# Kernel optimization log

Hardware: AMD Instinct MI355X
Metric: run time of the kernel (lower is better)

Reference implementation:

```python
import jax, jax.numpy as jnp
import numpy as np

BATCH = 4        # opt.batch_size
NPATCH = 4096    # patches per batch element
DIM = 256        # feature dim
MAXC = 5         # self.max_classes
T = 0.07         # opt.nce_T
NEG_FILL = -10.0


def setup_inputs() -> dict:
    key = jax.random.key(0)
    k1, k2, k3 = jax.random.split(key, 3)
    N = BATCH * NPATCH
    features_src = jax.random.normal(k1, (N, DIM), jnp.float32)
    features_tgt = jax.random.normal(k2, (N, DIM), jnp.float32)
    classes = jax.random.randint(k3, (N,), 0, MAXC, dtype=jnp.int32)
    return {"features_src": features_src, "features_tgt": features_tgt, "classes": classes}


def reference(features_src, features_tgt, classes):
    # feat_k = feat_k.detach()
    tgt = jax.lax.stop_gradient(features_tgt)

    # positive logits: per-row dot product, divided by temperature
    pos = jnp.sum(features_src * tgt, axis=-1) / T            # [N]

    src_b = features_src.reshape(BATCH, NPATCH, DIM)
    tgt_b = tgt.reshape(BATCH, NPATCH, DIM)
    cls = classes.reshape(BATCH, NPATCH)

    # full negative logit matrix per batch element
    logits = jnp.einsum('bnd,bmd->bnm', src_b, tgt_b)         # [B, n, n]
    same = cls[:, :, None] == cls[:, None, :]                 # [B, n, n] same-class mask

    # per-class smallest negative logit: min over (row in class c, col not in class c)
    row_min = jnp.min(jnp.where(same, jnp.inf, logits), axis=2)          # [B, n]
    class_eq = cls[:, :, None] == jnp.arange(MAXC)[None, None, :]        # [B, n, C]
    class_min = jnp.min(jnp.where(class_eq, row_min[:, :, None], jnp.inf), axis=1)  # [B, C]
    smallest = jnp.minimum(class_min, NEG_FILL) / T                      # [B, C]
    counts = jnp.sum(class_eq, axis=1)                                   # [B, C]

    # per-row pad value and pad multiplicity (num_pairs_should - num_pairs_is = count_c - 1)
    sm_row = jnp.take_along_axis(smallest, cls, axis=1)                  # [B, n]
    npad = jnp.take_along_axis(counts, cls, axis=1) - 1                  # [B, n]

    # logsumexp over [pos, negatives (other classes only), npad copies of smallest]
    lse_neg = jax.nn.logsumexp(jnp.where(same, -jnp.inf, logits / T), axis=2)  # [B, n]
    pad_term = jnp.where(npad > 0,
                         jnp.log(jnp.maximum(npad, 1).astype(jnp.float32)) + sm_row,
                         -jnp.inf)
    pos_b = pos.reshape(BATCH, NPATCH)
    lse = jax.nn.logsumexp(jnp.stack([pos_b, lse_neg, pad_term], axis=-1), axis=-1)
    loss = lse - pos_b                                                   # CE with label 0

    # match torch ordering: rows concatenated per batch, grouped by class (stable)
    order = jnp.argsort(cls, axis=1)  # jnp.argsort is stable
    return jnp.take_along_axis(loss, order, axis=1).reshape(-1)
```

## Files before the change

### kernel.cpp

```cpp
#include <hip/hip_runtime.h>
#include <cstdint>

#define NBATCH 4
#define NPATCH 4096
#define MAXC   5
#define BM 64
#define BN 64
#define NSPLIT 8
#define SPLITCOLS (NPATCH / NSPLIT)
#define NCIT (SPLITCOLS / BN)
#define SCALE  14.285714285714286f
#define SCALE2 20.609929006188747f
#define LN2F   0.6931471805599453f
#define NEGH  -1.0e38f
#define NEGFILL_T -142.85714285714286f
#define NROWS (NBATCH * NPATCH)

typedef __attribute__((ext_vector_type(8))) short short8;
typedef __attribute__((ext_vector_type(4))) float f32x4;

__device__ __forceinline__ float fexp2(float x) { return __builtin_amdgcn_exp2f(x); }
__device__ __forceinline__ float flog2(float x) { return __builtin_amdgcn_logf(x); }

__device__ __forceinline__ unsigned short f2bf(float f) {
  uint32_t u = __builtin_bit_cast(uint32_t, f);
  u = (u + 0x7FFFu + ((u >> 16) & 1u)) >> 16;
  return (unsigned short)u;
}


__global__ __launch_bounds__(256) void k_aux(const float* __restrict__ src,
                                             const float* __restrict__ tgt,
                                             const int* __restrict__ classes,
                                             unsigned short* __restrict__ tgtb,
                                             unsigned short* __restrict__ srcb,
                                             float* __restrict__ pos,
                                             int* __restrict__ outpos,
                                             int* __restrict__ counts) {
  int blk = blockIdx.x;
  if (blk < NROWS / 4) {
    int row  = blk * 4 + (threadIdx.x >> 6);
    int lane = threadIdx.x & 63;
    float4 va = ((const float4*)src)[(size_t)row * 64 + lane];
    float4 vb = ((const float4*)tgt)[(size_t)row * 64 + lane];
    float d = va.x * vb.x + va.y * vb.y + va.z * vb.z + va.w * vb.w;
#pragma unroll
    for (int off = 32; off > 0; off >>= 1) d += __shfl_xor(d, off, 64);
    if (lane == 0) pos[row] = d * SCALE;
    return;
  }
  if (blk < NROWS / 4 + 1024) {
    int which = (blk - NROWS / 4) >> 9;
    int fb = (blk - NROWS / 4) & 511;
    const float* in = which ? src : tgt;
    unsigned short* outb = which ? srcb : tgtb;
    float sc = which ? SCALE2 : 1.0f;
    int t  = threadIdx.x;
    int tl = fb * 2 + (t >> 7);
    int tt = t & 127;
    int row16 = tt >> 3;
    int kg    = tt & 7;
    const float4* rp = (const float4*)(in + (size_t)(tl * 16 + row16) * 256 + kg * 32);
    uint4* wp = (uint4*)outb + (size_t)tl * 512 + (size_t)(kg * 4) * 16 + row16;
#pragma unroll
    for (int j = 0; j < 4; ++j) {
      float4 fa = rp[j * 2];
      float4 fb2 = rp[j * 2 + 1];
      union { ushort4 h[2]; uint4 u; } pk;
      pk.h[0].x = f2bf(fa.x * sc);  pk.h[0].y = f2bf(fa.y * sc);
      pk.h[0].z = f2bf(fa.z * sc);  pk.h[0].w = f2bf(fa.w * sc);
      pk.h[1].x = f2bf(fb2.x * sc); pk.h[1].y = f2bf(fb2.y * sc);
      pk.h[1].z = f2bf(fb2.z * sc); pk.h[1].w = f2bf(fb2.w * sc);
      wp[j * 16] = pk.u;
    }
    return;
  }

  __shared__ int sa[MAXC * 256];
  __shared__ int sb2[MAXC * 256];
  int b = blk - (NROWS / 4 + 1024), t = threadIdx.x;
  int base = b * NPATCH + t * 16;
  int cv[16];
#pragma unroll
  for (int e = 0; e < 16; ++e) cv[e] = classes[base + e];
  int cnt[MAXC];
#pragma unroll
  for (int c = 0; c < MAXC; ++c) {
    cnt[c] = 0;
#pragma unroll
    for (int e = 0; e < 16; ++e)
      if (cv[e] == c) cnt[c]++;
  }
#pragma unroll
  for (int c = 0; c < MAXC; ++c) sa[c * 256 + t] = cnt[c];
  __syncthreads();

  int* rp = sa; int* wp = sb2;
  for (int d = 1; d < 256; d <<= 1) {
#pragma unroll
    for (int c = 0; c < MAXC; ++c) {
      int v = rp[c * 256 + t];
      if (t >= d) v += rp[c * 256 + t - d];
      wp[c * 256 + t] = v;
    }
    __syncthreads();
    int* tmp = rp; rp = wp; wp = tmp;
  }

  int tot[MAXC], excl[MAXC], off[MAXC + 1];
  off[0] = 0;
#pragma unroll
  for (int c = 0; c < MAXC; ++c) {
    tot[c]  = rp[c * 256 + 255];
    excl[c] = rp[c * 256 + t] - cnt[c];
    off[c + 1] = off[c] + tot[c];
  }
#pragma unroll
  for (int c = 0; c < MAXC; ++c) {
    int r = off[c] + excl[c];
#pragma unroll
    for (int e = 0; e < 16; ++e)
      if (cv[e] == c) { outpos[base + e] = r; r++; }
  }
  if (t < MAXC) counts[b * MAXC + t] = tot[t];
}

__global__ __launch_bounds__(256) void k_main(const unsigned short* __restrict__ srcb,
                                              const unsigned short* __restrict__ tgtb,
                                              const int* __restrict__ classes,
                                              float* __restrict__ pm,
                                              float* __restrict__ ps) {
  __shared__ float redm[2][BM], reds[2][BM];

  const int blk   = blockIdx.x;
  const int split = blk & (NSPLIT - 1);
  const int rbk   = blk >> 3;
  const int b     = rbk >> 6;
  const int rb    = rbk & 63;
  const int rowstart = b * NPATCH + rb * BM;
  const int tid = threadIdx.x;
  const int w = tid >> 6, lane = tid & 63, q = lane >> 4, l4 = lane & 15;
  const int rh = w >> 1, ch = w & 1;
  const int colbase = b * NPATCH + split * SPLITCOLS;

  const uint4* ap = (const uint4*)srcb + (size_t)(b * 256 + rb * 4 + rh * 2) * 512 + lane;
  uint4 afr[2][8];
#pragma unroll
  for (int rt = 0; rt < 2; ++rt)
#pragma unroll
    for (int ks = 0; ks < 8; ++ks)
      afr[rt][ks] = ap[rt * 512 + ks * 64];

  int rcls[2][4];
#pragma unroll
  for (int rt = 0; rt < 2; ++rt)
#pragma unroll
    for (int r = 0; r < 4; ++r)
      rcls[rt][r] = classes[rowstart + rh * 32 + rt * 16 + q * 4 + r];

  float m_[2][4], s_[2][4];
#pragma unroll
  for (int rt = 0; rt < 2; ++rt)
#pragma unroll
    for (int r = 0; r < 4; ++r) { m_[rt][r] = -INFINITY; s_[rt][r] = 0.f; }

  const uint4* bp = (const uint4*)tgtb
                  + (size_t)(b * 256 + split * 32 + ch * 2) * 512 + lane;
  const int* clp = classes + colbase + ch * 32 + l4;

  uint4 ea0[4], ea1[4], eb0[4], eb1[4];
#define LOADH(d0, d1, uoff)                                                         \
  {                                                                                 \
    _Pragma("unroll")                                                               \
    for (int i = 0; i < 4; ++i) {                                                   \
      d0[i] = bp[(uoff) + i * 64];                                                  \
      d1[i] = bp[(uoff) + i * 64 + 512];                                            \
    }                                                                               \
  }

#define STATS(ac, cc0, cc1)                                                         \
  {                                                                                 \
    _Pragma("unroll")                                                               \
    for (int rt = 0; rt < 2; ++rt) {                                                \
      _Pragma("unroll")                                                             \
      for (int r = 0; r < 4; ++r) {                                                 \
        int rc = rcls[rt][r];                                                       \
        float y0 = ((cc0) == rc) ? NEGH : (ac)[rt][0][r];                           \
        float y1 = ((cc1) == rc) ? NEGH : (ac)[rt][1][r];                           \
        float nm = fmaxf(m_[rt][r], fmaxf(y0, y1));                                 \
        float e01 = fexp2(y0 - nm) + fexp2(y1 - nm);                                \
        s_[rt][r] = fmaf(s_[rt][r], fexp2(m_[rt][r] - nm), e01);                    \
        m_[rt][r] = nm;                                                             \
      }                                                                             \
    }                                                                               \
  }

  LOADH(ea0, ea1, 0);

  f32x4 pacc[2][2];
  int pc0 = 0, pc1 = 0;

  for (int cit = 0; cit < NCIT; ++cit) {
    f32x4 acc[2][2];
#pragma unroll
    for (int rt = 0; rt < 2; ++rt)
#pragma unroll
      for (int ct = 0; ct < 2; ++ct) { f32x4 z = {0.f, 0.f, 0.f, 0.f}; acc[rt][ct] = z; }

    LOADH(eb0, eb1, cit * 2048 + 256);
    int c0 = clp[cit * 64];
    int c1 = clp[cit * 64 + 16];

#pragma unroll
    for (int ksl = 0; ksl < 4; ++ksl) {
      short8 b0 = __builtin_bit_cast(short8, ea0[ksl]);
      short8 b1 = __builtin_bit_cast(short8, ea1[ksl]);
#pragma unroll
      for (int rt = 0; rt < 2; ++rt) {
        short8 a = __builtin_bit_cast(short8, afr[rt][ksl]);
        acc[rt][0] = __builtin_amdgcn_mfma_f32_16x16x32_bf16(a, b0, acc[rt][0], 0, 0, 0);
        acc[rt][1] = __builtin_amdgcn_mfma_f32_16x16x32_bf16(a, b1, acc[rt][1], 0, 0, 0);
      }
    }

    if (cit + 1 < NCIT) LOADH(ea0, ea1, (cit + 1) * 2048);

    if (cit > 0) STATS(pacc, pc0, pc1);

#pragma unroll
    for (int ksl = 0; ksl < 4; ++ksl) {
      short8 b0 = __builtin_bit_cast(short8, eb0[ksl]);
      short8 b1 = __builtin_bit_cast(short8, eb1[ksl]);
#pragma unroll
      for (int rt = 0; rt < 2; ++rt) {
        short8 a = __builtin_bit_cast(short8, afr[rt][4 + ksl]);
        acc[rt][0] = __builtin_amdgcn_mfma_f32_16x16x32_bf16(a, b0, acc[rt][0], 0, 0, 0);
        acc[rt][1] = __builtin_amdgcn_mfma_f32_16x16x32_bf16(a, b1, acc[rt][1], 0, 0, 0);
      }
    }

#pragma unroll
    for (int rt = 0; rt < 2; ++rt)
#pragma unroll
      for (int ct = 0; ct < 2; ++ct) pacc[rt][ct] = acc[rt][ct];
    pc0 = c0; pc1 = c1;
  }
  STATS(pacc, pc0, pc1);
#undef LOADH
#undef STATS

#pragma unroll
  for (int off = 1; off < 16; off <<= 1) {
#pragma unroll
    for (int rt = 0; rt < 2; ++rt)
#pragma unroll
      for (int r = 0; r < 4; ++r) {
        float om = __shfl_xor(m_[rt][r], off, 64);
        float os = __shfl_xor(s_[rt][r], off, 64);
        float nm = fmaxf(m_[rt][r], om);
        s_[rt][r] = s_[rt][r] * fexp2(m_[rt][r] - nm) + os * fexp2(om - nm);
        m_[rt][r] = nm;
      }
  }

  if (l4 == 0) {
#pragma unroll
    for (int rt = 0; rt < 2; ++rt)
#pragma unroll
      for (int r = 0; r < 4; ++r) {
        int li = rh * 32 + rt * 16 + q * 4 + r;
        redm[ch][li] = m_[rt][r];
        reds[ch][li] = s_[rt][r];
      }
  }
  __syncthreads();
  if (tid < BM) {
    float m0 = redm[0][tid], m1 = redm[1][tid];
    float nm = fmaxf(m0, m1);
    float s  = reds[0][tid] * fexp2(m0 - nm) + reds[1][tid] * fexp2(m1 - nm);
    size_t o = (size_t)split * NROWS + rowstart + tid;
    pm[o] = nm;
    ps[o] = s;
  }
}

__global__ __launch_bounds__(256) void k_fin(const int* __restrict__ classes,
                                             const float* __restrict__ pos,
                                             const float* __restrict__ pm,
                                             const float* __restrict__ ps,
                                             const int* __restrict__ outpos,
                                             const int* __restrict__ counts,
                                             float* __restrict__ out) {
  int n = blockIdx.x * 256 + threadIdx.x;
  int b = n >> 12;
  int c = classes[n];
  float ps_ = pos[n];

  float M2 = -INFINITY;
  float mm[NSPLIT], ss[NSPLIT];
#pragma unroll
  for (int s = 0; s < NSPLIT; ++s) {
    mm[s] = pm[(size_t)s * NROWS + n];
    ss[s] = ps[(size_t)s * NROWS + n];
    M2 = fmaxf(M2, mm[s]);
  }
  float S2 = 0.f;
#pragma unroll
  for (int s = 0; s < NSPLIT; ++s) S2 = fmaf(ss[s], fexp2(mm[s] - M2), S2);
  float ln = (S2 > 0.f) ? (M2 + flog2(S2)) * LN2F : -INFINITY;

  int npad = counts[b * MAXC + c] - 1;
  float pt = (npad > 0) ? (logf((float)npad) + NEGFILL_T) : -INFINITY;
  float M = fmaxf(ps_, fmaxf(ln, pt));
  float lse = M + logf(expf(ps_ - M) + expf(ln - M) + expf(pt - M));
  out[b * NPATCH + outpos[n]] = lse - ps_;
}

extern "C" void kernel_launch(void* const* d_in, const int* in_sizes, int n_in,
                              void* d_out, int out_size, void* d_ws, size_t ws_size,
                              hipStream_t stream) {
  const float* src = (const float*)d_in[0];
  const float* tgt = (const float*)d_in[1];
  const int* cls   = (const int*)d_in[2];
  float* out = (float*)d_out;

  char* ws = (char*)d_ws;
  unsigned short* tgtb = (unsigned short*)(ws);
  unsigned short* srcb = (unsigned short*)(ws + 8388608);
  float* pos    = (float*)(ws + 16777216);
  float* pm     = (float*)(ws + 16842752);
  float* ps     = (float*)(ws + 17367040);
  int*   outpos = (int*)  (ws + 17891328);
  int*   counts = (int*)  (ws + 17956864);

  k_aux<<<NROWS / 4 + 1024 + NBATCH, 256, 0, stream>>>(src, tgt, cls, tgtb, srcb,
                                                       pos, outpos, counts);
  k_main<<<NBATCH * (NPATCH / BM) * NSPLIT, 256, 0, stream>>>(srcb, tgtb, cls, pm, ps);
  k_fin<<<NROWS / 256, 256, 0, stream>>>(cls, pos, pm, ps, outpos, counts, out);
}
```

Before: 139.6 us.

## Fuse positive dot product with bf16 conversion and ping-pong accumulators in main

```diff
diff --git a/kernel.cpp b/kernel.cpp
--- a/kernel.cpp
+++ b/kernel.cpp
@@ -38,47 +38,46 @@
                                              int* __restrict__ outpos,
                                              int* __restrict__ counts) {
   int blk = blockIdx.x;
-  if (blk < NROWS / 4) {
-    int row  = blk * 4 + (threadIdx.x >> 6);
-    int lane = threadIdx.x & 63;
-    float4 va = ((const float4*)src)[(size_t)row * 64 + lane];
-    float4 vb = ((const float4*)tgt)[(size_t)row * 64 + lane];
-    float d = va.x * vb.x + va.y * vb.y + va.z * vb.z + va.w * vb.w;
-#pragma unroll
-    for (int off = 32; off > 0; off >>= 1) d += __shfl_xor(d, off, 64);
-    if (lane == 0) pos[row] = d * SCALE;
-    return;
-  }
-  if (blk < NROWS / 4 + 1024) {
-    int which = (blk - NROWS / 4) >> 9;
-    int fb = (blk - NROWS / 4) & 511;
-    const float* in = which ? src : tgt;
-    unsigned short* outb = which ? srcb : tgtb;
-    float sc = which ? SCALE2 : 1.0f;
+  if (blk < 512) {
     int t  = threadIdx.x;
-    int tl = fb * 2 + (t >> 7);
+    int tl = blk * 2 + (t >> 7);
     int tt = t & 127;
     int row16 = tt >> 3;
     int kg    = tt & 7;
-    const float4* rp = (const float4*)(in + (size_t)(tl * 16 + row16) * 256 + kg * 32);
-    uint4* wp = (uint4*)outb + (size_t)tl * 512 + (size_t)(kg * 4) * 16 + row16;
+    size_t rowbase = (size_t)(tl * 16 + row16) * 256 + kg * 32;
+    const float4* rs = (const float4*)(src + rowbase);
+    const float4* rt_ = (const float4*)(tgt + rowbase);
+    uint4* wsrc = (uint4*)srcb + (size_t)tl * 512 + (size_t)(kg * 4) * 16 + row16;
+    uint4* wtgt = (uint4*)tgtb + (size_t)tl * 512 + (size_t)(kg * 4) * 16 + row16;
+    float d = 0.f;
 #pragma unroll
     for (int j = 0; j < 4; ++j) {
-      float4 fa = rp[j * 2];
-      float4 fb2 = rp[j * 2 + 1];
+      float4 sa = rs[j * 2], sb = rs[j * 2 + 1];
+      float4 ta = rt_[j * 2], tb = rt_[j * 2 + 1];
+      d += sa.x * ta.x + sa.y * ta.y + sa.z * ta.z + sa.w * ta.w
+         + sb.x * tb.x + sb.y * tb.y + sb.z * tb.z + sb.w * tb.w;
       union { ushort4 h[2]; uint4 u; } pk;
-      pk.h[0].x = f2bf(fa.x * sc);  pk.h[0].y = f2bf(fa.y * sc);
-      pk.h[0].z = f2bf(fa.z * sc);  pk.h[0].w = f2bf(fa.w * sc);
-      pk.h[1].x = f2bf(fb2.x * sc); pk.h[1].y = f2bf(fb2.y * sc);
-      pk.h[1].z = f2bf(fb2.z * sc); pk.h[1].w = f2bf(fb2.w * sc);
-      wp[j * 16] = pk.u;
-    }
+      pk.h[0].x = f2bf(sa.x * SCALE2); pk.h[0].y = f2bf(sa.y * SCALE2);
+      pk.h[0].z = f2bf(sa.z * SCALE2); pk.h[0].w = f2bf(sa.w * SCALE2);
+      pk.h[1].x = f2bf(sb.x * SCALE2); pk.h[1].y = f2bf(sb.y * SCALE2);
+      pk.h[1].z = f2bf(sb.z * SCALE2); pk.h[1].w = f2bf(sb.w * SCALE2);
+      wsrc[j * 16] = pk.u;
+      pk.h[0].x = f2bf(ta.x); pk.h[0].y = f2bf(ta.y);
+      pk.h[0].z = f2bf(ta.z); pk.h[0].w = f2bf(ta.w);
+      pk.h[1].x = f2bf(tb.x); pk.h[1].y = f2bf(tb.y);
+      pk.h[1].z = f2bf(tb.z); pk.h[1].w = f2bf(tb.w);
+      wtgt[j * 16] = pk.u;
+    }
+    d += __shfl_xor(d, 1, 64);
+    d += __shfl_xor(d, 2, 64);
+    d += __shfl_xor(d, 4, 64);
+    if (kg == 0) pos[tl * 16 + row16] = d * SCALE;
     return;
   }
 
   __shared__ int sa[MAXC * 256];
   __shared__ int sb2[MAXC * 256];
-  int b = blk - (NROWS / 4 + 1024), t = threadIdx.x;
+  int b = blk - 512, t = threadIdx.x;
   int base = b * NPATCH + t * 16;
   int cv[16];
 #pragma unroll
@@ -143,6 +142,19 @@
   const int rh = w >> 1, ch = w & 1;
   const int colbase = b * NPATCH + split * SPLITCOLS;
 
+  const uint4* bp = (const uint4*)tgtb
+                  + (size_t)(b * 256 + split * 32 + ch * 2) * 512 + lane;
+  const uint4* pA0 = bp;
+  const uint4* pA1 = bp + 512;
+  const uint4* pB0 = bp + 256;
+  const uint4* pB1 = bp + 768;
+  const int* clp = classes + colbase + ch * 32 + l4;
+
+  uint4 ea0[4], ea1[4], eb0[4], eb1[4];
+
+#pragma unroll
+  for (int i = 0; i < 4; ++i) { ea0[i] = pA0[i * 64]; ea1[i] = pA1[i * 64]; }
+
   const uint4* ap = (const uint4*)srcb + (size_t)(b * 256 + rb * 4 + rh * 2) * 512 + lane;
   uint4 afr[2][8];
 #pragma unroll
@@ -164,19 +176,9 @@
 #pragma unroll
     for (int r = 0; r < 4; ++r) { m_[rt][r] = -INFINITY; s_[rt][r] = 0.f; }
 
-  const uint4* bp = (const uint4*)tgtb
-                  + (size_t)(b * 256 + split * 32 + ch * 2) * 512 + lane;
-  const int* clp = classes + colbase + ch * 32 + l4;
-
-  uint4 ea0[4], ea1[4], eb0[4], eb1[4];
-#define LOADH(d0, d1, uoff)                                                         \
-  {                                                                                 \
-    _Pragma("unroll")                                                               \
-    for (int i = 0; i < 4; ++i) {                                                   \
-      d0[i] = bp[(uoff) + i * 64];                                                  \
-      d1[i] = bp[(uoff) + i * 64 + 512];                                            \
-    }                                                                               \
-  }
+  f32x4 zc = {0.f, 0.f, 0.f, 0.f};
+  f32x4 accs[2][2][2];
+  int pc0 = 0, pc1 = 0;
 
 #define STATS(ac, cc0, cc1)                                                         \
   {                                                                                 \
@@ -195,19 +197,14 @@
     }                                                                               \
   }
 
-  LOADH(ea0, ea1, 0);
-
-  f32x4 pacc[2][2];
-  int pc0 = 0, pc1 = 0;
-
+#pragma unroll
   for (int cit = 0; cit < NCIT; ++cit) {
-    f32x4 acc[2][2];
-#pragma unroll
-    for (int rt = 0; rt < 2; ++rt)
-#pragma unroll
-      for (int ct = 0; ct < 2; ++ct) { f32x4 z = {0.f, 0.f, 0.f, 0.f}; acc[rt][ct] = z; }
-
-    LOADH(eb0, eb1, cit * 2048 + 256);
+    f32x4 (*acc)[2] = accs[cit & 1];
+    f32x4 (*pac)[2] = accs[(cit & 1) ^ 1];
+
+#pragma unroll
+    for (int i = 0; i < 4; ++i) { eb0[i] = pB0[i * 64]; eb1[i] = pB1[i * 64]; }
+    pB0 += 2048; pB1 += 2048;
     int c0 = clp[cit * 64];
     int c1 = clp[cit * 64 + 16];
 
@@ -218,14 +215,20 @@
 #pragma unroll
       for (int rt = 0; rt < 2; ++rt) {
         short8 a = __builtin_bit_cast(short8, afr[rt][ksl]);
-        acc[rt][0] = __builtin_amdgcn_mfma_f32_16x16x32_bf16(a, b0, acc[rt][0], 0, 0, 0);
-        acc[rt][1] = __builtin_amdgcn_mfma_f32_16x16x32_bf16(a, b1, acc[rt][1], 0, 0, 0);
+        acc[rt][0] = __builtin_amdgcn_mfma_f32_16x16x32_bf16(
+            a, b0, (ksl == 0) ? zc : acc[rt][0], 0, 0, 0);
+        acc[rt][1] = __builtin_amdgcn_mfma_f32_16x16x32_bf16(
+            a, b1, (ksl == 0) ? zc : acc[rt][1], 0, 0, 0);
       }
     }
 
-    if (cit + 1 < NCIT) LOADH(ea0, ea1, (cit + 1) * 2048);
-
-    if (cit > 0) STATS(pacc, pc0, pc1);
+    if (cit + 1 < NCIT) {
+      pA0 += 2048; pA1 += 2048;
+#pragma unroll
+      for (int i = 0; i < 4; ++i) { ea0[i] = pA0[i * 64]; ea1[i] = pA1[i * 64]; }
+    }
+
+    if (cit > 0) STATS(pac, pc0, pc1);
 
 #pragma unroll
     for (int ksl = 0; ksl < 4; ++ksl) {
@@ -238,15 +241,9 @@
         acc[rt][1] = __builtin_amdgcn_mfma_f32_16x16x32_bf16(a, b1, acc[rt][1], 0, 0, 0);
       }
     }
-
-#pragma unroll
-    for (int rt = 0; rt < 2; ++rt)
-#pragma unroll
-      for (int ct = 0; ct < 2; ++ct) pacc[rt][ct] = acc[rt][ct];
     pc0 = c0; pc1 = c1;
   }
-  STATS(pacc, pc0, pc1);
-#undef LOADH
+  STATS(accs[(NCIT - 1) & 1], pc0, pc1);
 #undef STATS
 
 #pragma unroll
@@ -333,8 +330,7 @@
   int*   outpos = (int*)  (ws + 17891328);
   int*   counts = (int*)  (ws + 17956864);
 
-  k_aux<<<NROWS / 4 + 1024 + NBATCH, 256, 0, stream>>>(src, tgt, cls, tgtb, srcb,
-                                                       pos, outpos, counts);
+  k_aux<<<512 + NBATCH, 256, 0, stream>>>(src, tgt, cls, tgtb, srcb, pos, outpos, counts);
   k_main<<<NBATCH * (NPATCH / BM) * NSPLIT, 256, 0, stream>>>(srcb, tgtb, cls, pm, ps);
   k_fin<<<NROWS / 256, 256, 0, stream>>>(cls, pos, pm, ps, outpos, counts, out);
 }
```

Result: slower. 183.7 us (+31.5%).
